# Kernel tuning notes

Hardware: AMD Instinct MI355X
Metric: run time of the kernel (lower is better)

## Reference

```python
import jax, jax.numpy as jnp
import numpy as np
from jax import lax

B_, T_, C_ = 8, 1024, 768
H_, W_ = 32, 32
N_LAYER, LAYER_ID = 12, 5


def _fancy_init():
    # faithful 'fancy' init from Random_SpatialMix._init_weights
    r01 = LAYER_ID / (N_LAYER - 1)
    r1a0 = 1.0 - LAYER_ID / N_LAYER
    h = np.arange(C_, dtype=np.float64)
    decay = -5 + 8 * (h / (C_ - 1)) ** (0.7 + 1.3 * r01)
    zig = ((np.arange(C_) + 1) % 3 - 1) * 0.5
    first = np.log(0.3) + zig
    xlin = h / C_
    mix_k = xlin ** r1a0
    mix_v = xlin ** r1a0 + 0.3 * r01
    mix_r = xlin ** (0.5 * r1a0)
    f32 = lambda a: jnp.asarray(a, jnp.float32)
    return f32(decay), f32(first), f32(mix_k), f32(mix_v), f32(mix_r)


def setup_inputs() -> dict:
    key = jax.random.key(0)
    ks = jax.random.split(key, 6)
    s = 1.0 / np.sqrt(C_)
    x = jax.random.normal(ks[0], (B_, T_, C_), jnp.float32)
    Wk = jax.random.normal(ks[1], (C_, C_), jnp.float32) * s
    Wv = jax.random.normal(ks[2], (C_, C_), jnp.float32) * s
    Wr = jax.random.normal(ks[3], (C_, C_), jnp.float32) * s
    Wo = jax.random.normal(ks[4], (C_, C_), jnp.float32) * s
    decay, first, mk, mv, mr = _fancy_init()
    perm = jax.random.permutation(ks[5], C_).astype(jnp.int32)
    return dict(x=x, w_key=Wk, w_value=Wv, w_receptance=Wr, w_output=Wo,
                spatial_decay=decay, spatial_first=first,
                mix_k=mk, mix_v=mv, mix_r=mr, perm=perm, H=H_, W=W_)


def _shift2d(a, dh, dw, H, W):
    # zero-padded 2D shift of [B,H,W,g]
    pad = [(0, 0), (max(dh, 0), max(-dh, 0)), (max(dw, 0), max(-dw, 0)), (0, 0)]
    a = jnp.pad(a, pad)
    return a[:, max(-dh, 0):max(-dh, 0) + H, max(-dw, 0):max(-dw, 0) + W, :]


def q_shift(x, H, W, shift_pixel=1, gamma=0.25):
    # VRWKV q_shift: 4 channel groups shifted right/left/down/up, rest copied
    B, T, C = x.shape
    xi = x.reshape(B, H, W, C)
    g = int(C * gamma)
    parts = [
        _shift2d(xi[..., 0:g], 0, shift_pixel, H, W),
        _shift2d(xi[..., g:2 * g], 0, -shift_pixel, H, W),
        _shift2d(xi[..., 2 * g:3 * g], shift_pixel, 0, H, W),
        _shift2d(xi[..., 3 * g:4 * g], -shift_pixel, 0, H, W),
        xi[..., 4 * g:],
    ]
    return jnp.concatenate(parts, axis=-1).reshape(B, T, C)


def wkv(w, u, k, v):
    # RWKV-v4 WKV kernel (numerically stable form). w,u: [C]; k,v: [B,T,C]
    w = -jnp.exp(w)  # kernel applies w = -exp(w)
    B, T, C = k.shape

    def step(carry, kv):
        a, b, p = carry  # each [B,C]
        kt, vt = kv
        q = jnp.maximum(p, u + kt)
        e1 = jnp.exp(p - q)
        e2 = jnp.exp(u + kt - q)
        y = (e1 * a + e2 * vt) / (e1 * b + e2)
        q2 = jnp.maximum(p + w, kt)
        e1 = jnp.exp(p + w - q2)
        e2 = jnp.exp(kt - q2)
        return (e1 * a + e2 * vt, e1 * b + e2, q2), y

    init = (jnp.zeros((B, C), k.dtype), jnp.zeros((B, C), k.dtype),
            jnp.full((B, C), -1e38, k.dtype))
    _, y = lax.scan(step, init, (jnp.moveaxis(k, 1, 0), jnp.moveaxis(v, 1, 0)))
    return jnp.moveaxis(y, 0, 1)


def reference(x, w_key, w_value, w_receptance, w_output,
              spatial_decay, spatial_first, mix_k, mix_v, mix_r, perm, H, W):
    B, T, C = x.shape
    xx = q_shift(x, H, W)
    xk = x * mix_k + xx * (1 - mix_k)
    xv = x * mix_v + xx * (1 - mix_v)
    xr = x * mix_r + xx * (1 - mix_r)
    k = xk @ w_key.T
    v = xv @ w_value.T
    sr = jax.nn.sigmoid(xr @ w_receptance.T)
    # training path: shuffle CHANNEL axis (RevShuffle dim=2), run WKV, reverse
    ks_ = k[:, :, perm]
    vs_ = v[:, :, perm]
    wkv_s = wkv(spatial_decay / T, spatial_first / T, ks_, vs_)
    rev = jnp.zeros_like(perm).at[perm].set(jnp.arange(C, dtype=perm.dtype))
    wkv_out = wkv_s[:, :, rev]
    return (sr * wkv_out) @ w_output.T
```

## Files before the change

### kernel.cpp

```cpp
#include <hip/hip_runtime.h>
#include <hip/hip_bf16.h>
#include <stdint.h>

#define B_N 8
#define T_N 1024
#define C_N 768
#define M_N (B_N*T_N)
#define NCH 32
#define LCH (T_N/NCH)
#define BK  64

typedef __attribute__((ext_vector_type(4))) float f32x4;
typedef __attribute__((ext_vector_type(8))) short s16x8;
typedef __attribute__((ext_vector_type(4))) unsigned short u16x4;

__device__ __forceinline__ unsigned short f2bf(float f){
  unsigned int u = __float_as_uint(f);
  u += 0x7FFFu + ((u >> 16) & 1u);
  return (unsigned short)(u >> 16);
}

__device__ __forceinline__ void async16(const unsigned short* g, unsigned short* l){
  __builtin_amdgcn_global_load_lds(
      (const __attribute__((address_space(1))) unsigned int*)g,
      (__attribute__((address_space(3))) unsigned int*)l, 16, 0, 0);
}

__global__ __launch_bounds__(256) void prep_weights(
    const float* __restrict__ Wk, const float* __restrict__ Wv,
    const float* __restrict__ Wr, const float* __restrict__ Wo,
    const int* __restrict__ perm,
    unsigned short* __restrict__ Wkp, unsigned short* __restrict__ Wvp,
    unsigned short* __restrict__ Wrp, unsigned short* __restrict__ Wop)
{
  int idx = blockIdx.x*256 + threadIdx.x;
  int r = idx / C_N, c = idx - r*C_N;
  int pr = perm[r];
  Wkp[idx] = f2bf(Wk[pr*C_N + c]);
  Wvp[idx] = f2bf(Wv[pr*C_N + c]);
  Wrp[idx] = f2bf(Wr[pr*C_N + c]);
  Wop[idx] = f2bf(Wo[r*C_N + perm[c]]);
}

__global__ __launch_bounds__(256) void mix_kernel(
    const float* __restrict__ x,
    const float* __restrict__ mk, const float* __restrict__ mv, const float* __restrict__ mr,
    unsigned short* __restrict__ xk, unsigned short* __restrict__ xv, unsigned short* __restrict__ xr)
{
  int idx = blockIdx.x*256 + threadIdx.x;
  int n  = idx / (C_N/4);
  int c4 = (idx - n*(C_N/4)) * 4;
  int t = n & (T_N-1);
  int h = t >> 5, w = t & 31;
  int grp = c4 / 192;
  int dh = (grp==2) ? -1 : (grp==3) ? 1 : 0;
  int dw = (grp==0) ? -1 : (grp==1) ? 1 : 0;
  int h2 = h + dh, w2 = w + dw;
  bool valid = ((unsigned)h2 < 32u) && ((unsigned)w2 < 32u);
  f32x4 xc = *(const f32x4*)(x + (size_t)n*C_N + c4);
  f32x4 xx = {0.f,0.f,0.f,0.f};
  if (valid) xx = *(const f32x4*)(x + (size_t)(n + dh*32 + dw)*C_N + c4);
  f32x4 vk = *(const f32x4*)(mk + c4);
  f32x4 vv = *(const f32x4*)(mv + c4);
  f32x4 vr = *(const f32x4*)(mr + c4);
  u16x4 ok, ov, orr;
  #pragma unroll
  for (int i=0;i<4;++i){
    float d = xc[i] - xx[i];
    ok[i]  = f2bf(xx[i] + vk[i]*d);
    ov[i]  = f2bf(xx[i] + vv[i]*d);
    orr[i] = f2bf(xx[i] + vr[i]*d);
  }
  *(u16x4*)(xk + (size_t)n*C_N + c4) = ok;
  *(u16x4*)(xv + (size_t)n*C_N + c4) = ov;
  *(u16x4*)(xr + (size_t)n*C_N + c4) = orr;
}

__global__ __launch_bounds__(256) void gemm_kvr(
    const unsigned short* __restrict__ xk, const unsigned short* __restrict__ xv,
    const unsigned short* __restrict__ xr,
    const unsigned short* __restrict__ Wkp, const unsigned short* __restrict__ Wvp,
    const unsigned short* __restrict__ Wrp,
    float* __restrict__ kp, float* __restrict__ vp, float* __restrict__ srp)
{
  const int z = blockIdx.z;
  const unsigned short* A  = (z==0)? xk  : (z==1)? xv  : xr;
  const unsigned short* Bw = (z==0)? Wkp : (z==1)? Wvp : Wrp;
  const int m0 = blockIdx.x*128, n0 = blockIdx.y*128;
  __shared__ __align__(16) unsigned short As[128*BK];
  __shared__ __align__(16) unsigned short Bs[128*BK];
  const int tid = threadIdx.x;
  const int lane = tid & 63, wid = tid >> 6;
  const int wr = wid >> 1, wc = wid & 1;
  f32x4 acc[4][4];
  #pragma unroll
  for (int i=0;i<4;++i)
    #pragma unroll
    for (int j=0;j<4;++j) acc[i][j] = (f32x4){0.f,0.f,0.f,0.f};

  const int srow = tid >> 3;
  const int scol = (tid & 7) * 8;
  const int lr = lane & 15;
  const int lks = (lane >> 4) * 8;

  for (int k0 = 0; k0 < C_N; k0 += BK){
    #pragma unroll
    for (int it=0; it<4; ++it){
      int r = it*32 + srow;
      unsigned short* la = &As[(it*32 + wid*8)*BK];
      unsigned short* lb = &Bs[(it*32 + wid*8)*BK];
      async16(&A [(size_t)(m0+r)*C_N + k0 + scol], la);
      async16(&Bw[(size_t)(n0+r)*C_N + k0 + scol], lb);
    }
    __syncthreads();
    #pragma unroll
    for (int kk=0; kk<BK; kk+=32){
      const int lk = kk + lks;
      s16x8 af[4], bfr[4];
      #pragma unroll
      for (int mi=0;mi<4;++mi) af[mi]  = *(const s16x8*)&As[(wr*64 + mi*16 + lr)*BK + lk];
      #pragma unroll
      for (int ni=0;ni<4;++ni) bfr[ni] = *(const s16x8*)&Bs[(wc*64 + ni*16 + lr)*BK + lk];
      #pragma unroll
      for (int mi=0;mi<4;++mi)
        #pragma unroll
        for (int ni=0;ni<4;++ni)
          acc[mi][ni] = __builtin_amdgcn_mfma_f32_16x16x32_bf16(af[mi], bfr[ni], acc[mi][ni], 0,0,0);
    }
    __syncthreads();
  }
  const int lr4 = (lane>>4)*4, lc = lane & 15;
  #pragma unroll
  for (int mi=0;mi<4;++mi){
    #pragma unroll
    for (int ni=0;ni<4;++ni){
      #pragma unroll
      for (int i=0;i<4;++i){
        int m = m0 + wr*64 + mi*16 + lr4 + i;
        int n = n0 + wc*64 + ni*16 + lc;
        float val = acc[mi][ni][i];
        if (z==0)      kp[(size_t)m*C_N + n] = val;
        else if (z==1) vp[(size_t)m*C_N + n] = val;
        else           srp[(size_t)m*C_N + n] = 1.f/(1.f + __expf(-val));
      }
    }
  }
}

__global__ __launch_bounds__(256) void gemm_out(
    const unsigned short* __restrict__ A, const unsigned short* __restrict__ Bw,
    float* __restrict__ out)
{
  const int m0 = blockIdx.x*128, n0 = blockIdx.y*128;
  __shared__ __align__(16) unsigned short As[128*BK];
  __shared__ __align__(16) unsigned short Bs[128*BK];
  const int tid = threadIdx.x;
  const int lane = tid & 63, wid = tid >> 6;
  const int wr = wid >> 1, wc = wid & 1;
  f32x4 acc[4][4];
  #pragma unroll
  for (int i=0;i<4;++i)
    #pragma unroll
    for (int j=0;j<4;++j) acc[i][j] = (f32x4){0.f,0.f,0.f,0.f};

  const int srow = tid >> 3;
  const int scol = (tid & 7) * 8;
  const int lr = lane & 15;
  const int lks = (lane >> 4) * 8;

  for (int k0 = 0; k0 < C_N; k0 += BK){
    #pragma unroll
    for (int it=0; it<4; ++it){
      int r = it*32 + srow;
      unsigned short* la = &As[(it*32 + wid*8)*BK];
      unsigned short* lb = &Bs[(it*32 + wid*8)*BK];
      async16(&A [(size_t)(m0+r)*C_N + k0 + scol], la);
      async16(&Bw[(size_t)(n0+r)*C_N + k0 + scol], lb);
    }
    __syncthreads();
    #pragma unroll
    for (int kk=0; kk<BK; kk+=32){
      const int lk = kk + lks;
      s16x8 af[4], bfr[4];
      #pragma unroll
      for (int mi=0;mi<4;++mi) af[mi]  = *(const s16x8*)&As[(wr*64 + mi*16 + lr)*BK + lk];
      #pragma unroll
      for (int ni=0;ni<4;++ni) bfr[ni] = *(const s16x8*)&Bs[(wc*64 + ni*16 + lr)*BK + lk];
      #pragma unroll
      for (int mi=0;mi<4;++mi)
        #pragma unroll
        for (int ni=0;ni<4;++ni)
          acc[mi][ni] = __builtin_amdgcn_mfma_f32_16x16x32_bf16(af[mi], bfr[ni], acc[mi][ni], 0,0,0);
    }
    __syncthreads();
  }
  const int lr4 = (lane>>4)*4, lc = lane & 15;
  #pragma unroll
  for (int mi=0;mi<4;++mi)
    #pragma unroll
    for (int ni=0;ni<4;++ni)
      #pragma unroll
      for (int i=0;i<4;++i){
        int m = m0 + wr*64 + mi*16 + lr4 + i;
        int n = n0 + wc*64 + ni*16 + lc;
        out[(size_t)m*C_N + n] = acc[mi][ni][i];
      }
}

__global__ __launch_bounds__(256) void wkv_phase1(
    const float* __restrict__ kp, const float* __restrict__ vp,
    const float* __restrict__ decay,
    float* __restrict__ sa, float* __restrict__ sb, float* __restrict__ sp)
{
  int g = blockIdx.x*256 + threadIdx.x;
  int j = g % C_N;
  int cb = g / C_N;
  int b = cb % B_N, c = cb / B_N;
  float w = -__expf(decay[j] * (1.0f/T_N));
  float a = 0.f, bb = 0.f, p = -1e38f;
  size_t base = ((size_t)b*T_N + c*LCH)*C_N + j;
  #pragma unroll 4
  for (int t = 0; t < LCH; ++t){
    size_t o = base + (size_t)t*C_N;
    float kt = kp[o], vt = vp[o];
    float pw = p + w;
    float q2 = fmaxf(pw, kt);
    float e1 = __expf(pw - q2), e2 = __expf(kt - q2);
    a  = e1*a + e2*vt;
    bb = e1*bb + e2;
    p  = q2;
  }
  sa[g] = a; sb[g] = bb; sp[g] = p;
}

__global__ __launch_bounds__(256) void wkv_phase2(
    const float* __restrict__ decay,
    float* __restrict__ sa, float* __restrict__ sb, float* __restrict__ sp)
{
  int g = blockIdx.x*256 + threadIdx.x;
  int j = g % C_N, b = g / C_N;
  float w = -__expf(decay[j] * (1.0f/T_N));
  float wL = w * (float)LCH;
  float a = 0.f, bb = 0.f, p = -1e38f;
  for (int c = 0; c < NCH; ++c){
    size_t idx = ((size_t)c*B_N + b)*C_N + j;
    float la = sa[idx], lb = sb[idx], lp = sp[idx];
    sa[idx] = a; sb[idx] = bb; sp[idx] = p;
    float p1 = p + wL;
    float pn = fmaxf(p1, lp);
    float e1 = __expf(p1 - pn), e2 = __expf(lp - pn);
    a  = e1*a + e2*la;
    bb = e1*bb + e2*lb;
    p  = pn;
  }
}

__global__ __launch_bounds__(256) void wkv_phase3(
    const float* __restrict__ kp, const float* __restrict__ vp,
    const float* __restrict__ srp,
    const float* __restrict__ decay, const float* __restrict__ first,
    const float* __restrict__ sa, const float* __restrict__ sb,
    const float* __restrict__ sp,
    unsigned short* __restrict__ zp)
{
  int g = blockIdx.x*256 + threadIdx.x;
  int j = g % C_N;
  int cb = g / C_N;
  int b = cb % B_N, c = cb / B_N;
  float w = -__expf(decay[j] * (1.0f/T_N));
  float u = first[j] * (1.0f/T_N);
  float a = sa[g], bb = sb[g], p = sp[g];
  size_t base = ((size_t)b*T_N + c*LCH)*C_N + j;
  #pragma unroll 2
  for (int t = 0; t < LCH; ++t){
    size_t o = base + (size_t)t*C_N;
    float kt = kp[o], vt = vp[o];
    float uk = u + kt;
    float q  = fmaxf(p, uk);
    float e1 = __expf(p - q), e2 = __expf(uk - q);
    float y  = __fdividef(e1*a + e2*vt, e1*bb + e2);
    zp[o] = f2bf(srp[o] * y);
    float pw = p + w;
    float q2 = fmaxf(pw, kt);
    float e1b = __expf(pw - q2), e2b = __expf(kt - q2);
    a  = e1b*a + e2b*vt;
    bb = e1b*bb + e2b;
    p  = q2;
  }
}

extern "C" void kernel_launch(void* const* d_in, const int* in_sizes, int n_in,
                              void* d_out, int out_size, void* d_ws, size_t ws_size,
                              hipStream_t stream)
{
  const float* x     = (const float*)d_in[0];
  const float* Wk    = (const float*)d_in[1];
  const float* Wv    = (const float*)d_in[2];
  const float* Wr    = (const float*)d_in[3];
  const float* Wo    = (const float*)d_in[4];
  const float* decay = (const float*)d_in[5];
  const float* first = (const float*)d_in[6];
  const float* mk    = (const float*)d_in[7];
  const float* mv    = (const float*)d_in[8];
  const float* mr    = (const float*)d_in[9];
  const int*   perm  = (const int*)d_in[10];
  float* out = (float*)d_out;

  char* ws = (char*)d_ws;
  size_t off = 0;
  auto alloc = [&](size_t bytes)->char* {
    char* p = ws + off;
    off += (bytes + 255) & ~(size_t)255;
    return p;
  };
  const size_t MC = (size_t)M_N * C_N;
  const size_t CC = (size_t)C_N * C_N;
  const size_t SC = (size_t)NCH * B_N * C_N;
  unsigned short* xk  = (unsigned short*)alloc(MC*2);
  unsigned short* xv  = (unsigned short*)alloc(MC*2);
  unsigned short* xr  = (unsigned short*)alloc(MC*2);
  unsigned short* zp  = (unsigned short*)alloc(MC*2);
  unsigned short* Wkp = (unsigned short*)alloc(CC*2);
  unsigned short* Wvp = (unsigned short*)alloc(CC*2);
  unsigned short* Wrp = (unsigned short*)alloc(CC*2);
  unsigned short* Wop = (unsigned short*)alloc(CC*2);
  float* kp  = (float*)alloc(MC*4);
  float* vp  = (float*)alloc(MC*4);
  float* srp = (float*)alloc(MC*4);
  float* sa  = (float*)alloc(SC*4);
  float* sb  = (float*)alloc(SC*4);
  float* sp  = (float*)alloc(SC*4);

  prep_weights<<<dim3(CC/256), dim3(256), 0, stream>>>(Wk, Wv, Wr, Wo, perm,
                                                       Wkp, Wvp, Wrp, Wop);
  mix_kernel<<<dim3(MC/4/256), dim3(256), 0, stream>>>(x, mk, mv, mr, xk, xv, xr);
  gemm_kvr<<<dim3(M_N/128, C_N/128, 3), dim3(256), 0, stream>>>(
      xk, xv, xr, Wkp, Wvp, Wrp, kp, vp, srp);
  wkv_phase1<<<dim3(SC/256), dim3(256), 0, stream>>>(kp, vp, decay, sa, sb, sp);
  wkv_phase2<<<dim3(B_N*C_N/256), dim3(256), 0, stream>>>(decay, sa, sb, sp);
  wkv_phase3<<<dim3(SC/256), dim3(256), 0, stream>>>(kp, vp, srp, decay, first,
                                                     sa, sb, sp, zp);
  gemm_out<<<dim3(M_N/128, C_N/128), dim3(256), 0, stream>>>(zp, Wop, out);
}
```

Before: 135.4 us.

## Swizzle LDS tiles in GEMMs, concatenate KVR weights, store sigmoid(r) as bf16

Adds an XOR swizzle on the 16-byte column groups in both GEMMs' shared-memory tiles, applied on the async load and on the fragment reads, to cut LDS bank conflicts. The three K/V/R weight matrices now live in one concatenated buffer, and the z-dimension grid becomes a wider y-dimension grid. The sigmoid(r) output is stored as bf16 instead of fp32, halving that intermediate's write and read traffic in the WKV phase 3 kernel, with a small precision loss.

Result: faster. 131.3 us (-3.0%).

```diff
diff --git a/kernel.cpp b/kernel.cpp
--- a/kernel.cpp
+++ b/kernel.cpp
@@ -19,6 +19,9 @@
   u += 0x7FFFu + ((u >> 16) & 1u);
   return (unsigned short)(u >> 16);
 }
+__device__ __forceinline__ float bf2f(unsigned short h){
+  return __uint_as_float(((unsigned int)h) << 16);
+}
 
 __device__ __forceinline__ void async16(const unsigned short* g, unsigned short* l){
   __builtin_amdgcn_global_load_lds(
@@ -30,15 +33,15 @@
     const float* __restrict__ Wk, const float* __restrict__ Wv,
     const float* __restrict__ Wr, const float* __restrict__ Wo,
     const int* __restrict__ perm,
-    unsigned short* __restrict__ Wkp, unsigned short* __restrict__ Wvp,
-    unsigned short* __restrict__ Wrp, unsigned short* __restrict__ Wop)
+    unsigned short* __restrict__ Wall,
+    unsigned short* __restrict__ Wop)
 {
   int idx = blockIdx.x*256 + threadIdx.x;
   int r = idx / C_N, c = idx - r*C_N;
   int pr = perm[r];
-  Wkp[idx] = f2bf(Wk[pr*C_N + c]);
-  Wvp[idx] = f2bf(Wv[pr*C_N + c]);
-  Wrp[idx] = f2bf(Wr[pr*C_N + c]);
+  Wall[idx]            = f2bf(Wk[pr*C_N + c]);
+  Wall[idx +   (size_t)C_N*C_N] = f2bf(Wv[pr*C_N + c]);
+  Wall[idx + 2*(size_t)C_N*C_N] = f2bf(Wr[pr*C_N + c]);
   Wop[idx] = f2bf(Wo[r*C_N + perm[c]]);
 }
 
@@ -79,13 +82,79 @@
 __global__ __launch_bounds__(256) void gemm_kvr(
     const unsigned short* __restrict__ xk, const unsigned short* __restrict__ xv,
     const unsigned short* __restrict__ xr,
-    const unsigned short* __restrict__ Wkp, const unsigned short* __restrict__ Wvp,
-    const unsigned short* __restrict__ Wrp,
-    float* __restrict__ kp, float* __restrict__ vp, float* __restrict__ srp)
-{
-  const int z = blockIdx.z;
-  const unsigned short* A  = (z==0)? xk  : (z==1)? xv  : xr;
-  const unsigned short* Bw = (z==0)? Wkp : (z==1)? Wvp : Wrp;
+    const unsigned short* __restrict__ Wall,
+    float* __restrict__ kp, float* __restrict__ vp, unsigned short* __restrict__ srb)
+{
+  const int m0 = blockIdx.x*128, n0 = blockIdx.y*128;
+  const int z  = blockIdx.y / 6;
+  const unsigned short* A = (z==0)? xk : (z==1)? xv : xr;
+  __shared__ __align__(16) unsigned short As[128*BK];
+  __shared__ __align__(16) unsigned short Bs[128*BK];
+  const int tid = threadIdx.x;
+  const int lane = tid & 63, wid = tid >> 6;
+  const int wr = wid >> 1, wc = wid & 1;
+  f32x4 acc[4][4];
+  #pragma unroll
+  for (int i=0;i<4;++i)
+    #pragma unroll
+    for (int j=0;j<4;++j) acc[i][j] = (f32x4){0.f,0.f,0.f,0.f};
+
+  const int srow = tid >> 3;
+  const int scol = (((tid & 7) ^ ((tid >> 3) & 7)) * 8);
+  const int lr  = lane & 15;
+  const int x7  = lr & 7;
+  const int kh  = lane >> 4;
+
+  for (int k0 = 0; k0 < C_N; k0 += BK){
+    #pragma unroll
+    for (int it=0; it<4; ++it){
+      int r = it*32 + srow;
+      unsigned short* la = &As[(it*32 + wid*8)*BK];
+      unsigned short* lb = &Bs[(it*32 + wid*8)*BK];
+      async16(&A   [(size_t)(m0+r)*C_N + k0 + scol], la);
+      async16(&Wall[(size_t)(n0+r)*C_N + k0 + scol], lb);
+    }
+    __syncthreads();
+    #pragma unroll
+    for (int kk=0; kk<BK; kk+=32){
+      const int g = (kk>>3) + kh;
+      const int pg = (g ^ x7) << 3;
+      s16x8 af[4], bfr[4];
+      #pragma unroll
+      for (int mi=0;mi<4;++mi) af[mi]  = *(const s16x8*)&As[(wr*64 + mi*16 + lr)*BK + pg];
+      #pragma unroll
+      for (int ni=0;ni<4;++ni) bfr[ni] = *(const s16x8*)&Bs[(wc*64 + ni*16 + lr)*BK + pg];
+      #pragma unroll
+      for (int mi=0;mi<4;++mi)
+        #pragma unroll
+        for (int ni=0;ni<4;++ni)
+          acc[mi][ni] = __builtin_amdgcn_mfma_f32_16x16x32_bf16(af[mi], bfr[ni], acc[mi][ni], 0,0,0);
+    }
+    __syncthreads();
+  }
+  const int lr4 = (lane>>4)*4, lc = lane & 15;
+  const int colbase = n0 - z*C_N;
+  #pragma unroll
+  for (int mi=0;mi<4;++mi){
+    #pragma unroll
+    for (int ni=0;ni<4;++ni){
+      #pragma unroll
+      for (int i=0;i<4;++i){
+        int m = m0 + wr*64 + mi*16 + lr4 + i;
+        int n = colbase + wc*64 + ni*16 + lc;
+        float val = acc[mi][ni][i];
+        if (z==0)      kp[(size_t)m*C_N + n] = val;
+        else if (z==1) vp[(size_t)m*C_N + n] = val;
+        else           srb[(size_t)m*C_N + n] = f2bf(1.f/(1.f + __expf(-val)));
+      }
+    }
+  }
+}
+
+__global__ __launch_bounds__(256) void gemm_out(
+    const unsigned short* __restrict__ A, const unsigned short* __restrict__ Bw,
+    float* __restrict__ out)
+{
   const int m0 = blockIdx.x*128, n0 = blockIdx.y*128;
   __shared__ __align__(16) unsigned short As[128*BK];
   __shared__ __align__(16) unsigned short Bs[128*BK];
@@ -99,9 +168,10 @@
     for (int j=0;j<4;++j) acc[i][j] = (f32x4){0.f,0.f,0.f,0.f};
 
   const int srow = tid >> 3;
-  const int scol = (tid & 7) * 8;
-  const int lr = lane & 15;
-  const int lks = (lane >> 4) * 8;
+  const int scol = (((tid & 7) ^ ((tid >> 3) & 7)) * 8);
+  const int lr  = lane & 15;
+  const int x7  = lr & 7;
+  const int kh  = lane >> 4;
 
   for (int k0 = 0; k0 < C_N; k0 += BK){
     #pragma unroll
@@ -115,77 +185,13 @@
     __syncthreads();
     #pragma unroll
     for (int kk=0; kk<BK; kk+=32){
-      const int lk = kk + lks;
+      const int g = (kk>>3) + kh;
+      const int pg = (g ^ x7) << 3;
       s16x8 af[4], bfr[4];
       #pragma unroll
-      for (int mi=0;mi<4;++mi) af[mi]  = *(const s16x8*)&As[(wr*64 + mi*16 + lr)*BK + lk];
-      #pragma unroll
-      for (int ni=0;ni<4;++ni) bfr[ni] = *(const s16x8*)&Bs[(wc*64 + ni*16 + lr)*BK + lk];
-      #pragma unroll
-      for (int mi=0;mi<4;++mi)
-        #pragma unroll
-        for (int ni=0;ni<4;++ni)
-          acc[mi][ni] = __builtin_amdgcn_mfma_f32_16x16x32_bf16(af[mi], bfr[ni], acc[mi][ni], 0,0,0);
-    }
-    __syncthreads();
-  }
-  const int lr4 = (lane>>4)*4, lc = lane & 15;
-  #pragma unroll
-  for (int mi=0;mi<4;++mi){
-    #pragma unroll
-    for (int ni=0;ni<4;++ni){
-      #pragma unroll
-      for (int i=0;i<4;++i){
-        int m = m0 + wr*64 + mi*16 + lr4 + i;
-        int n = n0 + wc*64 + ni*16 + lc;
-        float val = acc[mi][ni][i];
-        if (z==0)      kp[(size_t)m*C_N + n] = val;
-        else if (z==1) vp[(size_t)m*C_N + n] = val;
-        else           srp[(size_t)m*C_N + n] = 1.f/(1.f + __expf(-val));
-      }
-    }
-  }
-}
-
-__global__ __launch_bounds__(256) void gemm_out(
-    const unsigned short* __restrict__ A, const unsigned short* __restrict__ Bw,
-    float* __restrict__ out)
-{
-  const int m0 = blockIdx.x*128, n0 = blockIdx.y*128;
-  __shared__ __align__(16) unsigned short As[128*BK];
-  __shared__ __align__(16) unsigned short Bs[128*BK];
-  const int tid = threadIdx.x;
-  const int lane = tid & 63, wid = tid >> 6;
-  const int wr = wid >> 1, wc = wid & 1;
-  f32x4 acc[4][4];
-  #pragma unroll
-  for (int i=0;i<4;++i)
-    #pragma unroll
-    for (int j=0;j<4;++j) acc[i][j] = (f32x4){0.f,0.f,0.f,0.f};
-
-  const int srow = tid >> 3;
-  const int scol = (tid & 7) * 8;
-  const int lr = lane & 15;
-  const int lks = (lane >> 4) * 8;
-
-  for (int k0 = 0; k0 < C_N; k0 += BK){
-    #pragma unroll
-    for (int it=0; it<4; ++it){
-      int r = it*32 + srow;
-      unsigned short* la = &As[(it*32 + wid*8)*BK];
-      unsigned short* lb = &Bs[(it*32 + wid*8)*BK];
-      async16(&A [(size_t)(m0+r)*C_N + k0 + scol], la);
-      async16(&Bw[(size_t)(n0+r)*C_N + k0 + scol], lb);
-    }
-    __syncthreads();
-    #pragma unroll
-    for (int kk=0; kk<BK; kk+=32){
-      const int lk = kk + lks;
-      s16x8 af[4], bfr[4];
-      #pragma unroll
-      for (int mi=0;mi<4;++mi) af[mi]  = *(const s16x8*)&As[(wr*64 + mi*16 + lr)*BK + lk];
-      #pragma unroll
-      for (int ni=0;ni<4;++ni) bfr[ni] = *(const s16x8*)&Bs[(wc*64 + ni*16 + lr)*BK + lk];
+      for (int mi=0;mi<4;++mi) af[mi]  = *(const s16x8*)&As[(wr*64 + mi*16 + lr)*BK + pg];
+      #pragma unroll
+      for (int ni=0;ni<4;++ni) bfr[ni] = *(const s16x8*)&Bs[(wc*64 + ni*16 + lr)*BK + pg];
       #pragma unroll
       for (int mi=0;mi<4;++mi)
         #pragma unroll
@@ -257,7 +263,7 @@
 
 __global__ __launch_bounds__(256) void wkv_phase3(
     const float* __restrict__ kp, const float* __restrict__ vp,
-    const float* __restrict__ srp,
+    const unsigned short* __restrict__ srb,
     const float* __restrict__ decay, const float* __restrict__ first,
     const float* __restrict__ sa, const float* __restrict__ sb,
     const float* __restrict__ sp,
@@ -279,7 +285,7 @@
     float q  = fmaxf(p, uk);
     float e1 = __expf(p - q), e2 = __expf(uk - q);
     float y  = __fdividef(e1*a + e2*vt, e1*bb + e2);
-    zp[o] = f2bf(srp[o] * y);
+    zp[o] = f2bf(bf2f(srb[o]) * y);
     float pw = p + w;
     float q2 = fmaxf(pw, kt);
     float e1b = __expf(pw - q2), e2b = __expf(kt - q2);
@@ -316,29 +322,27 @@
   const size_t MC = (size_t)M_N * C_N;
   const size_t CC = (size_t)C_N * C_N;
   const size_t SC = (size_t)NCH * B_N * C_N;
-  unsigned short* xk  = (unsigned short*)alloc(MC*2);
-  unsigned short* xv  = (unsigned short*)alloc(MC*2);
-  unsigned short* xr  = (unsigned short*)alloc(MC*2);
-  unsigned short* zp  = (unsigned short*)alloc(MC*2);
-  unsigned short* Wkp = (unsigned short*)alloc(CC*2);
-  unsigned short* Wvp = (unsigned short*)alloc(CC*2);
-  unsigned short* Wrp = (unsigned short*)alloc(CC*2);
-  unsigned short* Wop = (unsigned short*)alloc(CC*2);
+  unsigned short* xk   = (unsigned short*)alloc(MC*2);
+  unsigned short* xv   = (unsigned short*)alloc(MC*2);
+  unsigned short* xr   = (unsigned short*)alloc(MC*2);
+  unsigned short* zp   = (unsigned short*)alloc(MC*2);
+  unsigned short* Wall = (unsigned short*)alloc(CC*3*2);
+  unsigned short* Wop  = (unsigned short*)alloc(CC*2);
+  unsigned short* srb  = (unsigned short*)alloc(MC*2);
   float* kp  = (float*)alloc(MC*4);
   float* vp  = (float*)alloc(MC*4);
-  float* srp = (float*)alloc(MC*4);
   float* sa  = (float*)alloc(SC*4);
   float* sb  = (float*)alloc(SC*4);
   float* sp  = (float*)alloc(SC*4);
 
   prep_weights<<<dim3(CC/256), dim3(256), 0, stream>>>(Wk, Wv, Wr, Wo, perm,
-                                                       Wkp, Wvp, Wrp, Wop);
+                                                       Wall, Wop);
   mix_kernel<<<dim3(MC/4/256), dim3(256), 0, stream>>>(x, mk, mv, mr, xk, xv, xr);
-  gemm_kvr<<<dim3(M_N/128, C_N/128, 3), dim3(256), 0, stream>>>(
-      xk, xv, xr, Wkp, Wvp, Wrp, kp, vp, srp);
+  gemm_kvr<<<dim3(M_N/128, 3*C_N/128), dim3(256), 0, stream>>>(
+      xk, xv, xr, Wall, kp, vp, srb);
   wkv_phase1<<<dim3(SC/256), dim3(256), 0, stream>>>(kp, vp, decay, sa, sb, sp);
   wkv_phase2<<<dim3(B_N*C_N/256), dim3(256), 0, stream>>>(decay, sa, sb, sp);
-  wkv_phase3<<<dim3(SC/256), dim3(256), 0, stream>>>(kp, vp, srp, decay, first,
+  wkv_phase3<<<dim3(SC/256), dim3(256), 0, stream>>>(kp, vp, srb, decay, first,
                                                      sa, sb, sp, zp);
   gemm_out<<<dim3(M_N/128, C_N/128), dim3(256), 0, stream>>>(zp, Wop, out);
 }
```
